# Performance work log

Hardware: AMD Instinct MI355X
Metric: run time of the kernel (lower is better)

## Reference

```python
import jax, jax.numpy as jnp
import numpy as np

N, E = 50000, 1600000
IN, HID, HEADS, OUT = 128, 32, 4, 32
NEG_SLOPE = 0.2  # PyG GATConv default leaky_relu slope


def _glorot(k, shape):
    fan = shape[0] + shape[-1]
    return jax.random.normal(k, shape, dtype=jnp.float32) * np.sqrt(2.0 / fan).astype(np.float32)


def setup_inputs() -> dict:
    key = jax.random.key(0)
    ks = jax.random.split(key, 16)
    x = jax.random.normal(ks[0], (N, IN), dtype=jnp.float32)
    edge_index = jax.random.randint(ks[1], (2, E), 0, N, dtype=jnp.int32)
    # layer 0: in -> heads*hid, concat
    W0 = _glorot(ks[2], (IN, HEADS * HID))
    as0 = _glorot(ks[3], (HEADS, HID)); ad0 = _glorot(ks[4], (HEADS, HID))
    b0 = jnp.zeros((HEADS * HID,), jnp.float32)
    # layer 1: heads*hid -> heads*hid, concat
    W1 = _glorot(ks[5], (HEADS * HID, HEADS * HID))
    as1 = _glorot(ks[6], (HEADS, HID)); ad1 = _glorot(ks[7], (HEADS, HID))
    b1 = jnp.zeros((HEADS * HID,), jnp.float32)
    # layer 2: heads*hid -> out, heads=1, concat=False
    W2 = _glorot(ks[8], (HEADS * HID, OUT))
    as2 = _glorot(ks[9], (1, OUT)); ad2 = _glorot(ks[10], (1, OUT))
    b2 = jnp.zeros((OUT,), jnp.float32)
    return dict(x=x, edge_index=edge_index, W0=W0, as0=as0, ad0=ad0, b0=b0,
                W1=W1, as1=as1, ad1=ad1, b1=b1, W2=W2, as2=as2, ad2=ad2, b2=b2)


def gat_layer(x, src, dst, W, a_src, a_dst, b, heads, out_ch, concat):
    # linear transform per head: [N, heads, out_ch]
    h = (x @ W).reshape(N, heads, out_ch)
    # per-node attention half-logits: [N, heads]
    alpha_src = jnp.einsum('nhc,hc->nh', h, a_src)
    alpha_dst = jnp.einsum('nhc,hc->nh', h, a_dst)
    # per-edge logits (edge j -> i): [E', heads]
    logits = jax.nn.leaky_relu(alpha_src[src] + alpha_dst[dst], NEG_SLOPE)
    # segment softmax over incoming edges of each destination node
    m = jax.ops.segment_max(logits, dst, num_segments=N)
    e = jnp.exp(logits - m[dst])
    denom = jax.ops.segment_sum(e, dst, num_segments=N)
    alpha = e / denom[dst]
    # weighted message scatter-add: [N, heads, out_ch]
    out = jax.ops.segment_sum(h[src] * alpha[:, :, None], dst, num_segments=N)
    out = out.reshape(N, heads * out_ch) if concat else out.mean(axis=1)
    return out + b, alpha


def reference(x, edge_index, W0, as0, ad0, b0, W1, as1, ad1, b1, W2, as2, ad2, b2):
    # add self loops (PyG add_self_loops=True)
    loops = jnp.arange(N, dtype=edge_index.dtype)
    src = jnp.concatenate([edge_index[0], loops])
    dst = jnp.concatenate([edge_index[1], loops])

    h, alpha0 = gat_layer(x, src, dst, W0, as0, ad0, b0, HEADS, HID, True)
    h = jax.nn.elu(h)  # dropout inactive in eval mode
    h, _ = gat_layer(h, src, dst, W1, as1, ad1, b1, HEADS, HID, True)
    h = jax.nn.elu(h)
    out, _ = gat_layer(h, src, dst, W2, as2, ad2, b2, 1, OUT, False)
    return alpha0, out
```

## Files before the change

### kernel.cpp

```cpp
#include <hip/hip_runtime.h>
#include <math.h>

#define NN 50000
#define NEG 0.2f
#define TILE 4096

typedef __attribute__((ext_vector_type(8))) short short8;
typedef __attribute__((ext_vector_type(4))) float f32x4;

__device__ __forceinline__ unsigned short f2bf(float f){
    unsigned u = __float_as_uint(f);
    u += 0x7fffu + ((u >> 16) & 1u);
    return (unsigned short)(u >> 16);
}
__device__ __forceinline__ float bf2f(unsigned short v){
    return __uint_as_float(((unsigned)v) << 16);
}

__device__ __forceinline__ int excl_scan_256(int v, int* buf, int tid){
    buf[tid] = v;
    __syncthreads();
#pragma unroll
    for (int off = 1; off < 256; off <<= 1){
        int t = (tid >= off) ? buf[tid - off] : 0;
        __syncthreads();
        buf[tid] += t;
        __syncthreads();
    }
    return buf[tid] - v;
}

__global__ __launch_bounds__(256) void k_binning(const int* __restrict__ ei, int E,
        int* __restrict__ bucketCount, unsigned* __restrict__ tmp){
    __shared__ unsigned stage[TILE];
    __shared__ int hist[256], sbuf[256], exs[256], cur[256], gbase[256];
    int tid = threadIdx.x;
    int EP = E + NN;
    int tileBase = blockIdx.x * TILE;
    int cnt = min(TILE, EP - tileBase);

    hist[tid] = 0;
    __syncthreads();

    unsigned packed[16];
#pragma unroll
    for (int k = 0; k < 16; ++k){
        int e = tileBase + tid + (k << 8);
        unsigned p = 0xffffffffu;
        if (e < EP){
            int s, d;
            if (e < E){ s = ei[e]; d = ei[E + e]; } else { s = e - E; d = s; }
            p = ((unsigned)d << 16) | (unsigned)s;
            atomicAdd(&hist[d >> 8], 1);
        }
        packed[k] = p;
    }
    __syncthreads();
    int h = hist[tid];
    int ex = excl_scan_256(h, sbuf, tid);
    exs[tid] = ex;
    cur[tid] = ex;
    __syncthreads();
#pragma unroll
    for (int k = 0; k < 16; ++k){
        unsigned p = packed[k];
        if (p != 0xffffffffu){
            int b = p >> 24;
            int pos = atomicAdd(&cur[b], 1);
            stage[pos] = p;
        }
    }
    gbase[tid] = atomicAdd(&bucketCount[tid], h);
    __syncthreads();
    for (int i = tid; i < cnt; i += 256){
        unsigned p = stage[i];
        int b = p >> 24;
        tmp[(b << 14) + gbase[b] + (i - exs[b])] = p;
    }
}

__global__ __launch_bounds__(256) void k_bucket_csr(int EP,
        const int* __restrict__ bucketCount, const unsigned* __restrict__ tmp,
        int* __restrict__ row_ptr, unsigned short* __restrict__ ssrc){
    __shared__ int sbuf[256], deg[256], cur[256];
    __shared__ int baseSh, nSh;
    int b = blockIdx.x;
    int tid = threadIdx.x;
    int c = bucketCount[tid];
    int exb = excl_scan_256(c, sbuf, tid);
    if (tid == b){ baseSh = exb; nSh = c; }
    deg[tid] = 0;
    __syncthreads();
    int base = baseSh, n = nSh;
    const unsigned* tb = tmp + ((size_t)b << 14);
    for (int i = tid; i < n; i += 256)
        atomicAdd(&deg[(tb[i] >> 16) & 255], 1);
    __syncthreads();
    int d = deg[tid];
    int dx = excl_scan_256(d, sbuf, tid);
    cur[tid] = dx;
    int dst = (b << 8) + tid;
    if (dst < NN) row_ptr[dst] = base + dx;
    if (b == 0 && tid == 0) row_ptr[NN] = EP;
    __syncthreads();
    for (int i = tid; i < n; i += 256){
        unsigned p = tb[i];
        int pos = atomicAdd(&cur[(p >> 16) & 255], 1);
        ssrc[base + pos] = (unsigned short)(p & 0xffffu);
    }
}

__global__ void k_packW(const float* __restrict__ W0, const float* __restrict__ W1,
                        const float* __restrict__ W2,
                        unsigned short* __restrict__ h0, unsigned short* __restrict__ l0,
                        unsigned short* __restrict__ h1, unsigned short* __restrict__ l1,
                        unsigned short* __restrict__ h2, unsigned short* __restrict__ l2){
    int t = blockIdx.x * 256 + threadIdx.x;
    const float* W; unsigned short *ph, *pl; int Ncol; int u;
    if (t < 16384){ W = W0; ph = h0; pl = l0; Ncol = 128; u = t; }
    else if (t < 32768){ W = W1; ph = h1; pl = l1; Ncol = 128; u = t - 16384; }
    else if (t < 36864){ W = W2; ph = h2; pl = l2; Ncol = 32;  u = t - 32768; }
    else return;
    int n = u >> 7, k = u & 127;
    float f = W[k * Ncol + n];
    unsigned short hi = f2bf(f);
    unsigned short lo = f2bf(f - bf2f(hi));
    ph[n * 128 + k] = hi;
    pl[n * 128 + k] = lo;
}

template<int NT, int HH>
__global__ __launch_bounds__(256) void k_gemm_mfma(
        const float* __restrict__ A,
        const unsigned short* __restrict__ Bhi,
        const unsigned short* __restrict__ Blo,
        float* __restrict__ C, unsigned short* __restrict__ Cbf,
        const float* __restrict__ a_s,
        const float* __restrict__ a_d,
        float* __restrict__ asrc, float* __restrict__ adst, int M){
    const int Ncol = NT * 16;
    int wave = threadIdx.x >> 6;
    int lane = threadIdx.x & 63;
    int r    = lane & 15;
    int oct  = lane >> 4;
    int rowBase = blockIdx.x * 64 + wave * 16;

    f32x4 acc[NT];
#pragma unroll
    for (int c = 0; c < NT; ++c) acc[c] = (f32x4){0.f, 0.f, 0.f, 0.f};

    int lrow = rowBase + r; if (lrow > M - 1) lrow = M - 1;
    const float* arow = A + (size_t)lrow * 128;

    for (int t = 0; t < 4; ++t){
        int k0 = t * 32 + oct * 8;
        float4 a0 = *(const float4*)&arow[k0];
        float4 a1 = *(const float4*)&arow[k0 + 4];
        float av[8] = {a0.x, a0.y, a0.z, a0.w, a1.x, a1.y, a1.z, a1.w};
        short8 ahi, alo;
#pragma unroll
        for (int j = 0; j < 8; ++j){
            unsigned short h = f2bf(av[j]);
            unsigned short l = f2bf(av[j] - bf2f(h));
            ahi[j] = (short)h; alo[j] = (short)l;
        }
#pragma unroll
        for (int c = 0; c < NT; ++c){
            short8 bhi = *(const short8*)&Bhi[(c * 16 + r) * 128 + k0];
            short8 blo = *(const short8*)&Blo[(c * 16 + r) * 128 + k0];
            acc[c] = __builtin_amdgcn_mfma_f32_16x16x32_bf16(ahi, bhi, acc[c], 0, 0, 0);
            acc[c] = __builtin_amdgcn_mfma_f32_16x16x32_bf16(alo, bhi, acc[c], 0, 0, 0);
            acc[c] = __builtin_amdgcn_mfma_f32_16x16x32_bf16(ahi, blo, acc[c], 0, 0, 0);
        }
    }
#pragma unroll
    for (int c = 0; c < NT; ++c){
#pragma unroll
        for (int reg = 0; reg < 4; ++reg){
            int row = rowBase + oct * 4 + reg;
            if (row < M){
                int col = c * 16 + r;
                float v = acc[c][reg];
                if (C)   C[(size_t)row * Ncol + col] = v;
                if (Cbf) Cbf[(size_t)row * Ncol + col] = f2bf(v);
            }
        }
    }

    float as_v[NT], ad_v[NT];
#pragma unroll
    for (int c = 0; c < NT; ++c){
        as_v[c] = a_s[c * 16 + r];
        ad_v[c] = a_d[c * 16 + r];
    }
    float vs[HH * 4], vd[HH * 4];
#pragma unroll
    for (int h = 0; h < HH; ++h)
#pragma unroll
        for (int reg = 0; reg < 4; ++reg){
            vs[h * 4 + reg] = acc[2 * h][reg] * as_v[2 * h]
                            + acc[2 * h + 1][reg] * as_v[2 * h + 1];
            vd[h * 4 + reg] = acc[2 * h][reg] * ad_v[2 * h]
                            + acc[2 * h + 1][reg] * ad_v[2 * h + 1];
        }
#pragma unroll
    for (int off = 1; off < 16; off <<= 1){
#pragma unroll
        for (int k = 0; k < HH * 4; ++k){
            vs[k] += __shfl_xor(vs[k], off);
            vd[k] += __shfl_xor(vd[k], off);
        }
    }
    if (HH == 4){
        int reg = r & 3, hd = r >> 2;
        int row = rowBase + oct * 4 + reg;
        if (row < M){
            asrc[row * 4 + hd] = vs[hd * 4 + reg];
            adst[row * 4 + hd] = vd[hd * 4 + reg];
        }
    } else {
        int reg = r & 3;
        int row = rowBase + oct * 4 + reg;
        if (row < M){
            if (r < 4)       asrc[row] = vs[reg];
            else if (r < 8)  adst[row] = vd[reg];
        }
    }
}

__global__ __launch_bounds__(256) void k_agg4s(
        const uint4* __restrict__ hb4,
        const float* __restrict__ asrc, const float* __restrict__ adst,
        const int* __restrict__ row_ptr, const unsigned short* __restrict__ ssrc,
        const float* __restrict__ bias, float* __restrict__ outp,
        float* __restrict__ gdenom, int writeStats){
    int wave = (blockIdx.x * 256 + threadIdx.x) >> 6;
    int lane = threadIdx.x & 63;
    if (wave >= NN) return;
    int i = wave;
    int lo = row_ptr[i], hi = row_ptr[i + 1];
    int g = lane >> 4;
    int q = lane & 15;
    int myh = q >> 2;
    float adv = adst[i * 4 + myh];

    float acc[8];
#pragma unroll
    for (int k = 0; k < 8; ++k) acc[k] = 0.f;
    float dsum = 0.f;

#define AGG4_FMA(AA, GV) {                                                    \
        acc[0] += (AA) * __uint_as_float((GV).x << 16);                       \
        acc[1] += (AA) * __uint_as_float((GV).x & 0xffff0000u);               \
        acc[2] += (AA) * __uint_as_float((GV).y << 16);                       \
        acc[3] += (AA) * __uint_as_float((GV).y & 0xffff0000u);               \
        acc[4] += (AA) * __uint_as_float((GV).z << 16);                       \
        acc[5] += (AA) * __uint_as_float((GV).z & 0xffff0000u);               \
        acc[6] += (AA) * __uint_as_float((GV).w << 16);                       \
        acc[7] += (AA) * __uint_as_float((GV).w & 0xffff0000u); }
#define AGG4_ONE(JJ) {                                                        \
        float lg_ = asrc[(JJ) * 4u + myh] + adv;                              \
        lg_ = fmaxf(lg_, NEG * lg_);                                          \
        float a_ = __expf(lg_);                                               \
        dsum += a_;                                                           \
        uint4 gv_ = hb4[(JJ) * 16u + (unsigned)q];                            \
        AGG4_FMA(a_, gv_) }

    int idx = lo;
    if (lo & 1){
        if (g == 0){ unsigned j = ssrc[lo]; AGG4_ONE(j) }
        idx = lo + 1;
    }
    for (; idx + 8 <= hi; idx += 8){
        unsigned pair = *(const unsigned*)&ssrc[idx + 2 * g];
        unsigned j0 = pair & 0xffffu, j1 = pair >> 16;
        float s0 = asrc[j0 * 4u + myh];
        float s1 = asrc[j1 * 4u + myh];
        uint4 gv0 = hb4[j0 * 16u + (unsigned)q];
        uint4 gv1 = hb4[j1 * 16u + (unsigned)q];
        float lg0 = s0 + adv; lg0 = fmaxf(lg0, NEG * lg0);
        float lg1 = s1 + adv; lg1 = fmaxf(lg1, NEG * lg1);
        float a0 = __expf(lg0), a1 = __expf(lg1);
        dsum += a0 + a1;
        AGG4_FMA(a0, gv0)
        AGG4_FMA(a1, gv1)
    }
    {
        int k0 = idx + 2 * g, k1 = k0 + 1;
        if (k0 < hi){ unsigned j = ssrc[k0]; AGG4_ONE(j) }
        if (k1 < hi){ unsigned j = ssrc[k1]; AGG4_ONE(j) }
    }
#undef AGG4_ONE
#undef AGG4_FMA
#pragma unroll
    for (int k = 0; k < 8; ++k){
        acc[k] += __shfl_xor(acc[k], 16);
        acc[k] += __shfl_xor(acc[k], 32);
    }
    dsum += __shfl_xor(dsum, 16);
    dsum += __shfl_xor(dsum, 32);

    if (writeStats && g == 0 && (q & 3) == 0)
        gdenom[i * 4 + myh] = dsum;

    if (g == 0){
        float rs = 1.f / dsum;
        int c0 = q * 8;
        float4 bA = *(const float4*)&bias[c0];
        float4 bB = *(const float4*)&bias[c0 + 4];
        float o[8] = {acc[0] * rs + bA.x, acc[1] * rs + bA.y,
                      acc[2] * rs + bA.z, acc[3] * rs + bA.w,
                      acc[4] * rs + bB.x, acc[5] * rs + bB.y,
                      acc[6] * rs + bB.z, acc[7] * rs + bB.w};
#pragma unroll
        for (int k = 0; k < 8; ++k)
            o[k] = (o[k] > 0.f) ? o[k] : (__expf(o[k]) - 1.f);
        *(float4*)&outp[(size_t)i * 128 + c0]     = make_float4(o[0], o[1], o[2], o[3]);
        *(float4*)&outp[(size_t)i * 128 + c0 + 4] = make_float4(o[4], o[5], o[6], o[7]);
    }
}

__global__ void k_alpha0(const int* __restrict__ ei, int E,
                         const float4* __restrict__ asrc4, const float4* __restrict__ adst4,
                         const float4* __restrict__ gd4, float4* __restrict__ out){
    int e = blockIdx.x * 256 + threadIdx.x;
    int EP = E + NN;
    if (e >= EP) return;
    int s, d;
    if (e < E){ s = ei[e]; d = ei[E + e]; } else { s = e - E; d = s; }
    float4 as = asrc4[s], ad = adst4[d], dn = gd4[d];
    float4 r;
    float lg;
    lg = as.x + ad.x; lg = fmaxf(lg, NEG * lg); r.x = __expf(lg) / dn.x;
    lg = as.y + ad.y; lg = fmaxf(lg, NEG * lg); r.y = __expf(lg) / dn.y;
    lg = as.z + ad.z; lg = fmaxf(lg, NEG * lg); r.z = __expf(lg) / dn.z;
    lg = as.w + ad.w; lg = fmaxf(lg, NEG * lg); r.w = __expf(lg) / dn.w;
    out[e] = r;
}

__global__ __launch_bounds__(256) void k_agg1s(
        const float4* __restrict__ h24,
        const float* __restrict__ asrc, const float* __restrict__ adst,
        const int* __restrict__ row_ptr, const unsigned short* __restrict__ ssrc,
        const float* __restrict__ bias, float* __restrict__ outp){
    int wave = (blockIdx.x * 256 + threadIdx.x) >> 6;
    int lane = threadIdx.x & 63;
    if (wave >= NN) return;
    int i = wave;
    int lo = row_ptr[i], hi = row_ptr[i + 1];
    int g = lane >> 3;
    int q = lane & 7;
    float adv = adst[i];

    float acc[4] = {0.f, 0.f, 0.f, 0.f};
    float dsum = 0.f;

#define AGG1_ONE(JJ) {                                                        \
        float lg_ = asrc[(JJ)] + adv;                                         \
        lg_ = fmaxf(lg_, NEG * lg_);                                          \
        float a_ = __expf(lg_);                                               \
        dsum += a_;                                                           \
        float4 v_ = h24[(JJ) * 8u + (unsigned)q];                             \
        acc[0] += a_ * v_.x; acc[1] += a_ * v_.y;                             \
        acc[2] += a_ * v_.z; acc[3] += a_ * v_.w; }

    int idx = lo;
    if (lo & 1){
        if (g == 0){ unsigned j = ssrc[lo]; AGG1_ONE(j) }
        idx = lo + 1;
    }
    for (; idx + 16 <= hi; idx += 16){
        unsigned pair = *(const unsigned*)&ssrc[idx + 2 * g];
        unsigned j0 = pair & 0xffffu, j1 = pair >> 16;
        float s0 = asrc[j0];
        float s1 = asrc[j1];
        float4 v0 = h24[j0 * 8u + (unsigned)q];
        float4 v1 = h24[j1 * 8u + (unsigned)q];
        float lg0 = s0 + adv; lg0 = fmaxf(lg0, NEG * lg0);
        float lg1 = s1 + adv; lg1 = fmaxf(lg1, NEG * lg1);
        float a0 = __expf(lg0), a1 = __expf(lg1);
        dsum += a0 + a1;
        acc[0] += a0 * v0.x; acc[1] += a0 * v0.y;
        acc[2] += a0 * v0.z; acc[3] += a0 * v0.w;
        acc[0] += a1 * v1.x; acc[1] += a1 * v1.y;
        acc[2] += a1 * v1.z; acc[3] += a1 * v1.w;
    }
    {
        int k0 = idx + 2 * g, k1 = k0 + 1;
        if (k0 < hi){ unsigned j = ssrc[k0]; AGG1_ONE(j) }
        if (k1 < hi){ unsigned j = ssrc[k1]; AGG1_ONE(j) }
    }
#undef AGG1_ONE
#pragma unroll
    for (int k = 0; k < 4; ++k){
        acc[k] += __shfl_xor(acc[k], 8);
        acc[k] += __shfl_xor(acc[k], 16);
        acc[k] += __shfl_xor(acc[k], 32);
    }
    dsum += __shfl_xor(dsum, 8);
    dsum += __shfl_xor(dsum, 16);
    dsum += __shfl_xor(dsum, 32);
    if (g == 0){
        float rs = 1.f / dsum;
        float4 b = *(const float4*)&bias[q * 4];
        *(float4*)&outp[(size_t)i * 32 + q * 4] =
            make_float4(acc[0] * rs + b.x, acc[1] * rs + b.y,
                        acc[2] * rs + b.z, acc[3] * rs + b.w);
    }
}

extern "C" void kernel_launch(void* const* d_in, const int* in_sizes, int n_in,
                              void* d_out, int out_size, void* d_ws, size_t ws_size,
                              hipStream_t stream){
    const float* x   = (const float*)d_in[0];
    const int*   ei  = (const int*)  d_in[1];
    const float* W0  = (const float*)d_in[2];
    const float* as0 = (const float*)d_in[3];
    const float* ad0 = (const float*)d_in[4];
    const float* b0  = (const float*)d_in[5];
    const float* W1  = (const float*)d_in[6];
    const float* as1 = (const float*)d_in[7];
    const float* ad1 = (const float*)d_in[8];
    const float* b1  = (const float*)d_in[9];
    const float* W2  = (const float*)d_in[10];
    const float* as2 = (const float*)d_in[11];
    const float* ad2 = (const float*)d_in[12];
    const float* b2  = (const float*)d_in[13];

    const int E  = in_sizes[1] / 2;
    const int EP = E + NN;

    char* w = (char*)d_ws;
    size_t off = 0;
    auto carve = [&](size_t bytes) -> char* {
        char* p = w + off;
        off += (bytes + 255) & ~(size_t)255;
        return p;
    };
    int*            bucketCount = (int*)       carve(sizeof(int) * 256);
    int*            row_ptr = (int*)           carve(sizeof(int) * (NN + 1));
    unsigned short* ssrc    = (unsigned short*)carve(sizeof(short) * ((size_t)EP + 2));
    float*          hbuf    = (float*)         carve(sizeof(float) * (size_t)NN * 32);
    unsigned short* hb16    = (unsigned short*)carve(sizeof(short) * (size_t)NN * 128);
    float*          post    = (float*)         carve(sizeof(float) * (size_t)NN * 128);
    float*          asrc    = (float*)         carve(sizeof(float) * NN * 4);
    float*          adst    = (float*)         carve(sizeof(float) * NN * 4);
    float*          gdenom  = (float*)         carve(sizeof(float) * NN * 4);
    unsigned short* Whi0    = (unsigned short*)carve(sizeof(short) * 16384);
    unsigned short* Wlo0    = (unsigned short*)carve(sizeof(short) * 16384);
    unsigned short* Whi1    = (unsigned short*)carve(sizeof(short) * 16384);
    unsigned short* Wlo1    = (unsigned short*)carve(sizeof(short) * 16384);
    unsigned short* Whi2    = (unsigned short*)carve(sizeof(short) * 4096);
    unsigned short* Wlo2    = (unsigned short*)carve(sizeof(short) * 4096);
    unsigned*       tmp     = (unsigned*)post;

    float* out_alpha = (float*)d_out;
    float* out_final = (float*)d_out + (size_t)EP * 4;

    const int edgeBlocks = (EP + 255) / 256;
    const int waveBlocks = (NN + 3) / 4;
    const int gemmBlocks = (NN + 63) / 64;

    hipMemsetAsync(bucketCount, 0, sizeof(int) * 256, stream);
    k_binning   <<<(EP + TILE - 1) / TILE, 256, 0, stream>>>(ei, E, bucketCount, tmp);
    k_bucket_csr<<<256, 256, 0, stream>>>(EP, bucketCount, tmp, row_ptr, ssrc);
    k_packW     <<<144, 256, 0, stream>>>(W0, W1, W2, Whi0, Wlo0, Whi1, Wlo1, Whi2, Wlo2);

    k_gemm_mfma<8, 4><<<gemmBlocks, 256, 0, stream>>>(x, Whi0, Wlo0,
        nullptr, hb16, as0, ad0, asrc, adst, NN);
    k_agg4s<<<waveBlocks, 256, 0, stream>>>((const uint4*)hb16, asrc, adst, row_ptr,
                                            ssrc, b0, post, gdenom, 1);
    k_alpha0<<<edgeBlocks, 256, 0, stream>>>(ei, E, (const float4*)asrc, (const float4*)adst,
                                             (const float4*)gdenom, (float4*)out_alpha);

    k_gemm_mfma<8, 4><<<gemmBlocks, 256, 0, stream>>>(post, Whi1, Wlo1,
        nullptr, hb16, as1, ad1, asrc, adst, NN);
    k_agg4s<<<waveBlocks, 256, 0, stream>>>((const uint4*)hb16, asrc, adst, row_ptr,
                                            ssrc, b1, post, gdenom, 0);

    k_gemm_mfma<2, 1><<<gemmBlocks, 256, 0, stream>>>(post, Whi2, Wlo2,
        hbuf, nullptr, as2, ad2, asrc, adst, NN);
    k_agg1s<<<waveBlocks, 256, 0, stream>>>((const float4*)hbuf, asrc, adst, row_ptr,
                                            ssrc, b2, out_final);
}
```

Before: 412.1 us.

## Store bf16 features and attention logits head-major; aggregate one head per wave

The GEMM now writes the bf16 projected features and the per-node attention half-logits in head-major planes ([head][node][32] and [head][node]) instead of node-major. The aggregation kernel launches one wave per (head, node) pair, grouped by head, so consecutive waves gather from a single 3.2 MB feature plane. The aim is a smaller working set that stays in cache. The cost is four times as many waves, each re-reading the CSR row pointers and source indices, plus narrower 8-byte gathers per lane and an extra shuffle stage. k_alpha0 is adjusted to read the strided layout with four scalar loads per array.

```diff
diff --git a/kernel.cpp b/kernel.cpp
--- a/kernel.cpp
+++ b/kernel.cpp
@@ -179,10 +179,11 @@
         for (int reg = 0; reg < 4; ++reg){
             int row = rowBase + oct * 4 + reg;
             if (row < M){
-                int col = c * 16 + r;
+                int colg = c * 16 + r;
                 float v = acc[c][reg];
-                if (C)   C[(size_t)row * Ncol + col] = v;
-                if (Cbf) Cbf[(size_t)row * Ncol + col] = f2bf(v);
+                if (C)   C[(size_t)row * Ncol + colg] = v;
+                if (Cbf) Cbf[(size_t)(colg >> 5) * ((size_t)M * 32)
+                             + (size_t)row * 32 + (colg & 31)] = f2bf(v);
             }
         }
     }
@@ -215,8 +216,8 @@
         int reg = r & 3, hd = r >> 2;
         int row = rowBase + oct * 4 + reg;
         if (row < M){
-            asrc[row * 4 + hd] = vs[hd * 4 + reg];
-            adst[row * 4 + hd] = vd[hd * 4 + reg];
+            asrc[hd * M + row] = vs[hd * 4 + reg];
+            adst[hd * M + row] = vd[hd * 4 + reg];
         }
     } else {
         int reg = r & 3;
@@ -228,113 +229,111 @@
     }
 }
 
-__global__ __launch_bounds__(256) void k_agg4s(
-        const uint4* __restrict__ hb4,
-        const float* __restrict__ asrc, const float* __restrict__ adst,
+__global__ __launch_bounds__(256) void k_aggh(
+        const unsigned short* __restrict__ hb,
+        const float* __restrict__ asrc,
+        const float* __restrict__ adst,
         const int* __restrict__ row_ptr, const unsigned short* __restrict__ ssrc,
         const float* __restrict__ bias, float* __restrict__ outp,
         float* __restrict__ gdenom, int writeStats){
-    int wave = (blockIdx.x * 256 + threadIdx.x) >> 6;
+    int wid = (blockIdx.x * 256 + threadIdx.x) >> 6;
+    if (wid >= 4 * NN) return;
     int lane = threadIdx.x & 63;
-    if (wave >= NN) return;
-    int i = wave;
+    int h = wid / NN;
+    int i = wid - h * NN;
+    int g = lane >> 3;
+    int q = lane & 7;
     int lo = row_ptr[i], hi = row_ptr[i + 1];
-    int g = lane >> 4;
-    int q = lane & 15;
-    int myh = q >> 2;
-    float adv = adst[i * 4 + myh];
-
-    float acc[8];
-#pragma unroll
-    for (int k = 0; k < 8; ++k) acc[k] = 0.f;
+    float adv = adst[h * NN + i];
+    const unsigned short* hp = hb + (size_t)h * (NN * 32);
+    const float* ap = asrc + h * NN;
+
+    float acc[4] = {0.f, 0.f, 0.f, 0.f};
     float dsum = 0.f;
 
-#define AGG4_FMA(AA, GV) {                                                    \
-        acc[0] += (AA) * __uint_as_float((GV).x << 16);                       \
-        acc[1] += (AA) * __uint_as_float((GV).x & 0xffff0000u);               \
-        acc[2] += (AA) * __uint_as_float((GV).y << 16);                       \
-        acc[3] += (AA) * __uint_as_float((GV).y & 0xffff0000u);               \
-        acc[4] += (AA) * __uint_as_float((GV).z << 16);                       \
-        acc[5] += (AA) * __uint_as_float((GV).z & 0xffff0000u);               \
-        acc[6] += (AA) * __uint_as_float((GV).w << 16);                       \
-        acc[7] += (AA) * __uint_as_float((GV).w & 0xffff0000u); }
-#define AGG4_ONE(JJ) {                                                        \
-        float lg_ = asrc[(JJ) * 4u + myh] + adv;                              \
+#define AGH_FMA(AA, VV) {                                                     \
+        acc[0] += (AA) * __uint_as_float((VV).x << 16);                       \
+        acc[1] += (AA) * __uint_as_float((VV).x & 0xffff0000u);               \
+        acc[2] += (AA) * __uint_as_float((VV).y << 16);                       \
+        acc[3] += (AA) * __uint_as_float((VV).y & 0xffff0000u); }
+#define AGH_ONE(JJ) {                                                         \
+        float lg_ = ap[(JJ)] + adv;                                           \
         lg_ = fmaxf(lg_, NEG * lg_);                                          \
         float a_ = __expf(lg_);                                               \
         dsum += a_;                                                           \
-        uint4 gv_ = hb4[(JJ) * 16u + (unsigned)q];                            \
-        AGG4_FMA(a_, gv_) }
+        uint2 v_ = *(const uint2*)&hp[(JJ) * 32u + (unsigned)(q * 4)];        \
+        AGH_FMA(a_, v_) }
 
     int idx = lo;
     if (lo & 1){
-        if (g == 0){ unsigned j = ssrc[lo]; AGG4_ONE(j) }
+        if (g == 0){ unsigned j = ssrc[lo]; AGH_ONE(j) }
         idx = lo + 1;
     }
-    for (; idx + 8 <= hi; idx += 8){
+    for (; idx + 16 <= hi; idx += 16){
         unsigned pair = *(const unsigned*)&ssrc[idx + 2 * g];
         unsigned j0 = pair & 0xffffu, j1 = pair >> 16;
-        float s0 = asrc[j0 * 4u + myh];
-        float s1 = asrc[j1 * 4u + myh];
-        uint4 gv0 = hb4[j0 * 16u + (unsigned)q];
-        uint4 gv1 = hb4[j1 * 16u + (unsigned)q];
+        float s0 = ap[j0];
+        float s1 = ap[j1];
+        uint2 v0 = *(const uint2*)&hp[j0 * 32u + (unsigned)(q * 4)];
+        uint2 v1 = *(const uint2*)&hp[j1 * 32u + (unsigned)(q * 4)];
         float lg0 = s0 + adv; lg0 = fmaxf(lg0, NEG * lg0);
         float lg1 = s1 + adv; lg1 = fmaxf(lg1, NEG * lg1);
         float a0 = __expf(lg0), a1 = __expf(lg1);
         dsum += a0 + a1;
-        AGG4_FMA(a0, gv0)
-        AGG4_FMA(a1, gv1)
+        AGH_FMA(a0, v0)
+        AGH_FMA(a1, v1)
     }
     {
         int k0 = idx + 2 * g, k1 = k0 + 1;
-        if (k0 < hi){ unsigned j = ssrc[k0]; AGG4_ONE(j) }
-        if (k1 < hi){ unsigned j = ssrc[k1]; AGG4_ONE(j) }
-    }
-#undef AGG4_ONE
-#undef AGG4_FMA
-#pragma unroll
-    for (int k = 0; k < 8; ++k){
+        if (k0 < hi){ unsigned j = ssrc[k0]; AGH_ONE(j) }
+        if (k1 < hi){ unsigned j = ssrc[k1]; AGH_ONE(j) }
+    }
+#undef AGH_ONE
+#undef AGH_FMA
+#pragma unroll
+    for (int k = 0; k < 4; ++k){
+        acc[k] += __shfl_xor(acc[k], 8);
         acc[k] += __shfl_xor(acc[k], 16);
         acc[k] += __shfl_xor(acc[k], 32);
     }
+    dsum += __shfl_xor(dsum, 8);
     dsum += __shfl_xor(dsum, 16);
     dsum += __shfl_xor(dsum, 32);
 
-    if (writeStats && g == 0 && (q & 3) == 0)
-        gdenom[i * 4 + myh] = dsum;
+    if (writeStats && lane == 0)
+        gdenom[i * 4 + h] = dsum;
 
     if (g == 0){
         float rs = 1.f / dsum;
-        int c0 = q * 8;
-        float4 bA = *(const float4*)&bias[c0];
-        float4 bB = *(const float4*)&bias[c0 + 4];
-        float o[8] = {acc[0] * rs + bA.x, acc[1] * rs + bA.y,
-                      acc[2] * rs + bA.z, acc[3] * rs + bA.w,
-                      acc[4] * rs + bB.x, acc[5] * rs + bB.y,
-                      acc[6] * rs + bB.z, acc[7] * rs + bB.w};
-#pragma unroll
-        for (int k = 0; k < 8; ++k)
-            o[k] = (o[k] > 0.f) ? o[k] : (__expf(o[k]) - 1.f);
-        *(float4*)&outp[(size_t)i * 128 + c0]     = make_float4(o[0], o[1], o[2], o[3]);
-        *(float4*)&outp[(size_t)i * 128 + c0 + 4] = make_float4(o[4], o[5], o[6], o[7]);
+        int c0 = h * 32 + q * 4;
+        float4 b = *(const float4*)&bias[c0];
+        float o0 = acc[0] * rs + b.x;
+        float o1 = acc[1] * rs + b.y;
+        float o2 = acc[2] * rs + b.z;
+        float o3 = acc[3] * rs + b.w;
+        o0 = (o0 > 0.f) ? o0 : (__expf(o0) - 1.f);
+        o1 = (o1 > 0.f) ? o1 : (__expf(o1) - 1.f);
+        o2 = (o2 > 0.f) ? o2 : (__expf(o2) - 1.f);
+        o3 = (o3 > 0.f) ? o3 : (__expf(o3) - 1.f);
+        *(float4*)&outp[(size_t)i * 128 + c0] = make_float4(o0, o1, o2, o3);
     }
 }
 
 __global__ void k_alpha0(const int* __restrict__ ei, int E,
-                         const float4* __restrict__ asrc4, const float4* __restrict__ adst4,
+                         const float* __restrict__ asrc, const float* __restrict__ adst,
                          const float4* __restrict__ gd4, float4* __restrict__ out){
     int e = blockIdx.x * 256 + threadIdx.x;
     int EP = E + NN;
     if (e >= EP) return;
     int s, d;
     if (e < E){ s = ei[e]; d = ei[E + e]; } else { s = e - E; d = s; }
-    float4 as = asrc4[s], ad = adst4[d], dn = gd4[d];
+    float4 dn = gd4[d];
     float4 r;
     float lg;
-    lg = as.x + ad.x; lg = fmaxf(lg, NEG * lg); r.x = __expf(lg) / dn.x;
-    lg = as.y + ad.y; lg = fmaxf(lg, NEG * lg); r.y = __expf(lg) / dn.y;
-    lg = as.z + ad.z; lg = fmaxf(lg, NEG * lg); r.z = __expf(lg) / dn.z;
-    lg = as.w + ad.w; lg = fmaxf(lg, NEG * lg); r.w = __expf(lg) / dn.w;
+    lg = asrc[s]          + adst[d];          lg = fmaxf(lg, NEG * lg); r.x = __expf(lg) / dn.x;
+    lg = asrc[NN + s]     + adst[NN + d];     lg = fmaxf(lg, NEG * lg); r.y = __expf(lg) / dn.y;
+    lg = asrc[2 * NN + s] + adst[2 * NN + d]; lg = fmaxf(lg, NEG * lg); r.z = __expf(lg) / dn.z;
+    lg = asrc[3 * NN + s] + adst[3 * NN + d]; lg = fmaxf(lg, NEG * lg); r.w = __expf(lg) / dn.w;
     out[e] = r;
 }
 
@@ -459,6 +458,7 @@
 
     const int edgeBlocks = (EP + 255) / 256;
     const int waveBlocks = (NN + 3) / 4;
+    const int aggBlocks  = NN;
     const int gemmBlocks = (NN + 63) / 64;
 
     hipMemsetAsync(bucketCount, 0, sizeof(int) * 256, stream);
@@ -468,15 +468,15 @@
 
     k_gemm_mfma<8, 4><<<gemmBlocks, 256, 0, stream>>>(x, Whi0, Wlo0,
         nullptr, hb16, as0, ad0, asrc, adst, NN);
-    k_agg4s<<<waveBlocks, 256, 0, stream>>>((const uint4*)hb16, asrc, adst, row_ptr,
-                                            ssrc, b0, post, gdenom, 1);
-    k_alpha0<<<edgeBlocks, 256, 0, stream>>>(ei, E, (const float4*)asrc, (const float4*)adst,
+    k_aggh<<<aggBlocks, 256, 0, stream>>>(hb16, asrc, adst, row_ptr,
+                                          ssrc, b0, post, gdenom, 1);
+    k_alpha0<<<edgeBlocks, 256, 0, stream>>>(ei, E, asrc, adst,
                                              (const float4*)gdenom, (float4*)out_alpha);
 
     k_gemm_mfma<8, 4><<<gemmBlocks, 256, 0, stream>>>(post, Whi1, Wlo1,
         nullptr, hb16, as1, ad1, asrc, adst, NN);
-    k_agg4s<<<waveBlocks, 256, 0, stream>>>((const uint4*)hb16, asrc, adst, row_ptr,
-                                            ssrc, b1, post, gdenom, 0);
+    k_aggh<<<aggBlocks, 256, 0, stream>>>(hb16, asrc, adst, row_ptr,
+                                          ssrc, b1, post, gdenom, 0);
 
     k_gemm_mfma<2, 1><<<gemmBlocks, 256, 0, stream>>>(post, Whi2, Wlo2,
         hbuf, nullptr, as2, ad2, asrc, adst, NN);
```

After: 542.2 us. 1.32x slower.

## Aggregate final GAT layer from bf16 features with four nodes per wave

Applied to the files above, without the earlier changes.

The last layer's projected features are now stored as bf16 instead of fp32, which halves the bytes gathered per edge. The aggregation kernel now packs four destination nodes into each wave, using 16 lanes per node and 4 edge groups with 8 channels per lane. The main loop is unrolled to four edges per lane, adding memory-level parallelism. In exchange the layer-2 messages lose precision from bf16 rounding, and lanes within a wave may sit idle when the degrees of its four nodes differ.

```diff
diff --git a/kernel.cpp b/kernel.cpp
--- a/kernel.cpp
+++ b/kernel.cpp
@@ -338,74 +338,111 @@
     out[e] = r;
 }
 
-__global__ __launch_bounds__(256) void k_agg1s(
-        const float4* __restrict__ h24,
+__global__ __launch_bounds__(256) void k_agg1b(
+        const uint4* __restrict__ hb,
         const float* __restrict__ asrc, const float* __restrict__ adst,
         const int* __restrict__ row_ptr, const unsigned short* __restrict__ ssrc,
         const float* __restrict__ bias, float* __restrict__ outp){
-    int wave = (blockIdx.x * 256 + threadIdx.x) >> 6;
+    int wave = threadIdx.x >> 6;
     int lane = threadIdx.x & 63;
-    if (wave >= NN) return;
-    int i = wave;
-    int lo = row_ptr[i], hi = row_ptr[i + 1];
-    int g = lane >> 3;
-    int q = lane & 7;
-    float adv = adst[i];
-
-    float acc[4] = {0.f, 0.f, 0.f, 0.f};
+    int ns = lane >> 4;
+    int g  = (lane >> 2) & 3;
+    int q  = lane & 3;
+    int i  = blockIdx.x * 16 + wave * 4 + ns;
+    bool valid = (i < NN);
+    int iv = valid ? i : NN - 1;
+    int lo = row_ptr[iv], hi = row_ptr[iv + 1];
+    float adv = adst[iv];
+
+    float acc[8];
+#pragma unroll
+    for (int k = 0; k < 8; ++k) acc[k] = 0.f;
     float dsum = 0.f;
 
-#define AGG1_ONE(JJ) {                                                        \
+#define AGB_FMA(AA, GV) {                                                     \
+        acc[0] += (AA) * __uint_as_float((GV).x << 16);                       \
+        acc[1] += (AA) * __uint_as_float((GV).x & 0xffff0000u);               \
+        acc[2] += (AA) * __uint_as_float((GV).y << 16);                       \
+        acc[3] += (AA) * __uint_as_float((GV).y & 0xffff0000u);               \
+        acc[4] += (AA) * __uint_as_float((GV).z << 16);                       \
+        acc[5] += (AA) * __uint_as_float((GV).z & 0xffff0000u);               \
+        acc[6] += (AA) * __uint_as_float((GV).w << 16);                       \
+        acc[7] += (AA) * __uint_as_float((GV).w & 0xffff0000u); }
+#define AGB_ONE(JJ) {                                                         \
         float lg_ = asrc[(JJ)] + adv;                                         \
         lg_ = fmaxf(lg_, NEG * lg_);                                          \
         float a_ = __expf(lg_);                                               \
         dsum += a_;                                                           \
-        float4 v_ = h24[(JJ) * 8u + (unsigned)q];                             \
-        acc[0] += a_ * v_.x; acc[1] += a_ * v_.y;                             \
-        acc[2] += a_ * v_.z; acc[3] += a_ * v_.w; }
+        uint4 gv_ = hb[(JJ) * 4u + (unsigned)q];                              \
+        AGB_FMA(a_, gv_) }
 
     int idx = lo;
     if (lo & 1){
-        if (g == 0){ unsigned j = ssrc[lo]; AGG1_ONE(j) }
+        if (g == 0){ unsigned j = ssrc[lo]; AGB_ONE(j) }
         idx = lo + 1;
     }
     for (; idx + 16 <= hi; idx += 16){
-        unsigned pair = *(const unsigned*)&ssrc[idx + 2 * g];
-        unsigned j0 = pair & 0xffffu, j1 = pair >> 16;
-        float s0 = asrc[j0];
-        float s1 = asrc[j1];
-        float4 v0 = h24[j0 * 8u + (unsigned)q];
-        float4 v1 = h24[j1 * 8u + (unsigned)q];
+        unsigned pA = *(const unsigned*)&ssrc[idx + 2 * g];
+        unsigned pB = *(const unsigned*)&ssrc[idx + 8 + 2 * g];
+        unsigned j0 = pA & 0xffffu, j1 = pA >> 16;
+        unsigned j2 = pB & 0xffffu, j3 = pB >> 16;
+        float s0 = asrc[j0], s1 = asrc[j1], s2 = asrc[j2], s3 = asrc[j3];
+        uint4 v0 = hb[j0 * 4u + (unsigned)q];
+        uint4 v1 = hb[j1 * 4u + (unsigned)q];
+        uint4 v2 = hb[j2 * 4u + (unsigned)q];
+        uint4 v3 = hb[j3 * 4u + (unsigned)q];
+        float lg0 = s0 + adv; lg0 = fmaxf(lg0, NEG * lg0);
+        float lg1 = s1 + adv; lg1 = fmaxf(lg1, NEG * lg1);
+        float lg2 = s2 + adv; lg2 = fmaxf(lg2, NEG * lg2);
+        float lg3 = s3 + adv; lg3 = fmaxf(lg3, NEG * lg3);
+        float a0 = __expf(lg0), a1 = __expf(lg1);
+        float a2 = __expf(lg2), a3 = __expf(lg3);
+        dsum += (a0 + a1) + (a2 + a3);
+        AGB_FMA(a0, v0)
+        AGB_FMA(a1, v1)
+        AGB_FMA(a2, v2)
+        AGB_FMA(a3, v3)
+    }
+    if (idx + 8 <= hi){
+        unsigned pA = *(const unsigned*)&ssrc[idx + 2 * g];
+        unsigned j0 = pA & 0xffffu, j1 = pA >> 16;
+        float s0 = asrc[j0], s1 = asrc[j1];
+        uint4 v0 = hb[j0 * 4u + (unsigned)q];
+        uint4 v1 = hb[j1 * 4u + (unsigned)q];
         float lg0 = s0 + adv; lg0 = fmaxf(lg0, NEG * lg0);
         float lg1 = s1 + adv; lg1 = fmaxf(lg1, NEG * lg1);
         float a0 = __expf(lg0), a1 = __expf(lg1);
         dsum += a0 + a1;
-        acc[0] += a0 * v0.x; acc[1] += a0 * v0.y;
-        acc[2] += a0 * v0.z; acc[3] += a0 * v0.w;
-        acc[0] += a1 * v1.x; acc[1] += a1 * v1.y;
-        acc[2] += a1 * v1.z; acc[3] += a1 * v1.w;
+        AGB_FMA(a0, v0)
+        AGB_FMA(a1, v1)
+        idx += 8;
     }
     {
         int k0 = idx + 2 * g, k1 = k0 + 1;
-        if (k0 < hi){ unsigned j = ssrc[k0]; AGG1_ONE(j) }
-        if (k1 < hi){ unsigned j = ssrc[k1]; AGG1_ONE(j) }
-    }
-#undef AGG1_ONE
-#pragma unroll
-    for (int k = 0; k < 4; ++k){
+        if (k0 < hi){ unsigned j = ssrc[k0]; AGB_ONE(j) }
+        if (k1 < hi){ unsigned j = ssrc[k1]; AGB_ONE(j) }
+    }
+#undef AGB_ONE
+#undef AGB_FMA
+#pragma unroll
+    for (int k = 0; k < 8; ++k){
+        acc[k] += __shfl_xor(acc[k], 4);
         acc[k] += __shfl_xor(acc[k], 8);
-        acc[k] += __shfl_xor(acc[k], 16);
-        acc[k] += __shfl_xor(acc[k], 32);
-    }
+    }
+    dsum += __shfl_xor(dsum, 4);
     dsum += __shfl_xor(dsum, 8);
-    dsum += __shfl_xor(dsum, 16);
-    dsum += __shfl_xor(dsum, 32);
-    if (g == 0){
+
+    if (g == 0 && valid){
         float rs = 1.f / dsum;
-        float4 b = *(const float4*)&bias[q * 4];
-        *(float4*)&outp[(size_t)i * 32 + q * 4] =
-            make_float4(acc[0] * rs + b.x, acc[1] * rs + b.y,
-                        acc[2] * rs + b.z, acc[3] * rs + b.w);
+        int c0 = q * 8;
+        float4 bA = *(const float4*)&bias[c0];
+        float4 bB = *(const float4*)&bias[c0 + 4];
+        *(float4*)&outp[(size_t)i * 32 + c0] =
+            make_float4(acc[0] * rs + bA.x, acc[1] * rs + bA.y,
+                        acc[2] * rs + bA.z, acc[3] * rs + bA.w);
+        *(float4*)&outp[(size_t)i * 32 + c0 + 4] =
+            make_float4(acc[4] * rs + bB.x, acc[5] * rs + bB.y,
+                        acc[6] * rs + bB.z, acc[7] * rs + bB.w);
     }
 }
 
@@ -440,7 +477,7 @@
     int*            bucketCount = (int*)       carve(sizeof(int) * 256);
     int*            row_ptr = (int*)           carve(sizeof(int) * (NN + 1));
     unsigned short* ssrc    = (unsigned short*)carve(sizeof(short) * ((size_t)EP + 2));
-    float*          hbuf    = (float*)         carve(sizeof(float) * (size_t)NN * 32);
+    unsigned short* hb2     = (unsigned short*)carve(sizeof(short) * (size_t)NN * 32);
     unsigned short* hb16    = (unsigned short*)carve(sizeof(short) * (size_t)NN * 128);
     float*          post    = (float*)         carve(sizeof(float) * (size_t)NN * 128);
     float*          asrc    = (float*)         carve(sizeof(float) * NN * 4);
@@ -459,6 +496,7 @@
 
     const int edgeBlocks = (EP + 255) / 256;
     const int waveBlocks = (NN + 3) / 4;
+    const int agg1Blocks = (NN + 15) / 16;
     const int gemmBlocks = (NN + 63) / 64;
 
     hipMemsetAsync(bucketCount, 0, sizeof(int) * 256, stream);
@@ -479,7 +517,7 @@
                                             ssrc, b1, post, gdenom, 0);
 
     k_gemm_mfma<2, 1><<<gemmBlocks, 256, 0, stream>>>(post, Whi2, Wlo2,
-        hbuf, nullptr, as2, ad2, asrc, adst, NN);
-    k_agg1s<<<waveBlocks, 256, 0, stream>>>((const float4*)hbuf, asrc, adst, row_ptr,
+        nullptr, hb2, as2, ad2, asrc, adst, NN);
+    k_agg1b<<<agg1Blocks, 256, 0, stream>>>((const uint4*)hb2, asrc, adst, row_ptr,
                                             ssrc, b2, out_final);
 }
```

After: 399.6 us. 3.0% less time.
